# Performance work log

Hardware: AMD Instinct MI355X
Metric: run time of the kernel (lower is better)

Reference implementation:

```python
import jax, jax.numpy as jnp
import numpy as np

V = 32000   # vocab.size
E = 512     # embed_dim
H = 512     # hidden_dim
L = 2       # num_layers
W = 32      # window_size
S = 512     # seq_len
B = 8       # batch


def setup_inputs() -> dict:
    key = jax.random.key(0)
    ks = jax.random.split(key, 2 + 4 * L)
    bound = 1.0 / np.sqrt(H)
    inp = {
        "encoder_input": jax.random.randint(ks[0], (S, B), 0, V),
        "embed_table": jax.random.normal(ks[1], (V, E), jnp.float32),
    }
    for l in range(L):
        in_dim = E if l == 0 else H
        k = ks[2 + 4 * l: 6 + 4 * l]
        inp[f"w_ih_{l}"] = jax.random.uniform(k[0], (4 * H, in_dim), jnp.float32, -bound, bound)
        inp[f"w_hh_{l}"] = jax.random.uniform(k[1], (4 * H, H), jnp.float32, -bound, bound)
        inp[f"b_ih_{l}"] = jax.random.uniform(k[2], (4 * H,), jnp.float32, -bound, bound)
        inp[f"b_hh_{l}"] = jax.random.uniform(k[3], (4 * H,), jnp.float32, -bound, bound)
    return inp


def _lstm_layer(x, mask, w_ih, w_hh, b_ih, b_hh):
    # x: [T, N, D]; mask: [T, N, 1]. Masked steps keep (h, c), so every window
    # effectively starts from a zero state at its first valid position (same as
    # running a fresh LSTM on each window, torch gate order i,f,g,o).
    N = x.shape[1]
    Hd = w_hh.shape[1]
    bias = b_ih + b_hh

    def step(carry, inp_):
        h, c = carry
        xt, mt = inp_
        gates = xt @ w_ih.T + h @ w_hh.T + bias  # [N, 4H]
        i, f, g, o = jnp.split(gates, 4, axis=-1)
        i = jax.nn.sigmoid(i)
        f = jax.nn.sigmoid(f)
        g = jnp.tanh(g)
        o = jax.nn.sigmoid(o)
        c_new = f * c + i * g
        h_new = o * jnp.tanh(c_new)
        h = jnp.where(mt, h_new, h)
        c = jnp.where(mt, c_new, c)
        return (h, c), h

    z = jnp.zeros((N, Hd), x.dtype)
    (h, _), ys = jax.lax.scan(step, (z, z), (x, mask))
    return ys, h


def reference(encoder_input, embed_table,
              w_ih_0, w_hh_0, b_ih_0, b_hh_0,
              w_ih_1, w_hh_1, b_ih_1, b_hh_1):
    emb = embed_table[encoder_input]              # [S, B, E]
    T = W + 1
    # window position t for target index i is i - W + t (invalid when < 0)
    pos = jnp.arange(S)[None, :] - W + jnp.arange(T)[:, None]  # [T, S]
    valid = pos >= 0
    windows = emb[jnp.clip(pos, 0)]               # [T, S, B, E]
    x = windows.reshape(T, S * B, E)
    mask = jnp.broadcast_to(valid[:, :, None], (T, S, B)).reshape(T, S * B, 1)

    params = [(w_ih_0, w_hh_0, b_ih_0, b_hh_0), (w_ih_1, w_hh_1, b_ih_1, b_hh_1)]
    h = None
    for (wi, wh, bi, bh) in params:
        x, h = _lstm_layer(x, mask, wi, wh, bi, bh)
    # original takes encoder_output at the last window position == final hidden
    return h.reshape(S, B, H)
```

## Files before the change

### kernel.cpp

```cpp
#include <hip/hip_runtime.h>
#include <stdint.h>

#define NROWS 4096
#define HDIM  512
#define GDIM  2048
#define WWIN  32

typedef __attribute__((ext_vector_type(8))) short short8;
typedef __attribute__((ext_vector_type(4))) float f32x4;

__device__ __forceinline__ unsigned short f2bf(float x){
  union { float f; unsigned int u; } v; v.f = x;
  unsigned int u = v.u + 0x7fffu + ((v.u >> 16) & 1u);
  return (unsigned short)(u >> 16);
}

__device__ __forceinline__ void gld16(const void* g, void* l){
  __builtin_amdgcn_global_load_lds(
      (const __attribute__((address_space(1))) unsigned int*)g,
      (__attribute__((address_space(3))) unsigned int*)l, 16, 0, 0);
}

__device__ __forceinline__ float sigm(float x){ return 1.f/(1.f + __expf(-x)); }
__device__ __forceinline__ float tanh_f(float x){ return 1.f - 2.f/(1.f + __expf(2.f*x)); }

__device__ __forceinline__ void gemm_tile_db(
    const char* A0, const char* A1, const char* Bsrc,
    int ldbB, int nk, int r0, int c0,
    char* smem, int wr, int wc, int lane, f32x4 acc[4][4])
{
  const int tid = threadIdx.x;
  const int oo0 = tid * 16;
  const int srow = oo0 >> 7;
  const int scb  = oo0 & 127;
  const size_t aOff = (size_t)(r0 + srow) * 1024 + scb;
  const size_t bOff = (size_t)(c0 + srow) * (size_t)ldbB + scb;

  auto STAGE = [&](int kk, int buf){
    const char* Ap = (kk < 8) ? A0 : A1;
    const size_t kbA = (size_t)(kk & 7) * 128;
    const size_t kbB = (size_t)kk * 128;
    char* AsB = smem + buf * 16384;
    char* BsB = smem + 32768 + buf * 16384;
    #pragma unroll
    for (int i = 0; i < 4; ++i){
      const size_t rstep = (size_t)i * 32;
      gld16(Ap   + aOff + rstep * 1024          + kbA, AsB + i*4096 + oo0);
      gld16(Bsrc + bOff + rstep * (size_t)ldbB  + kbB, BsB + i*4096 + oo0);
    }
  };

  STAGE(0, 0);
  __syncthreads();

  const int lr = lane & 15;
  const int lk = (lane >> 4) * 8;

  for (int kk = 0; kk < nk; ++kk){
    const int cur = kk & 1;
    if (kk + 1 < nk) STAGE(kk + 1, cur ^ 1);

    const unsigned short* As = (const unsigned short*)(smem + cur*16384);
    const unsigned short* Bs = (const unsigned short*)(smem + 32768 + cur*16384);
    short8 a[2][4], b[2][4];
    #pragma unroll
    for (int h = 0; h < 2; ++h){
      const int k32 = h * 32;
      #pragma unroll
      for (int m = 0; m < 4; ++m)
        a[h][m] = *(const short8*)(As + (64*wr + 16*m + lr)*64 + k32 + lk);
      #pragma unroll
      for (int n = 0; n < 4; ++n)
        b[h][n] = *(const short8*)(Bs + (64*wc + 16*n + lr)*64 + k32 + lk);
    }
    __builtin_amdgcn_s_setprio(1);
    #pragma unroll
    for (int h = 0; h < 2; ++h)
      #pragma unroll
      for (int m = 0; m < 4; ++m)
        #pragma unroll
        for (int n = 0; n < 4; ++n)
          acc[m][n] = __builtin_amdgcn_mfma_f32_16x16x32_bf16(a[h][m], b[h][n], acc[m][n], 0, 0, 0);
    __builtin_amdgcn_s_setprio(0);

    __syncthreads();
  }
}

__global__ void __launch_bounds__(256) prep_weights(
    const float* wih0, const float* whh0, const float* bih0, const float* bhh0,
    const float* wih1, const float* whh1, const float* bih1, const float* bhh1,
    unsigned short* BrIh0, unsigned short* Br0, unsigned short* Br1,
    float* bias0r, float* br1)
{
  const int j = blockIdx.x;
  const int g = j & 3, hd = j >> 2;
  const int r = g*512 + hd;
  for (int k = threadIdx.x; k < 512; k += 256){
    BrIh0[(size_t)j*512 + k]      = f2bf(wih0[(size_t)r*512 + k]);
    Br0  [(size_t)j*512 + k]      = f2bf(whh0[(size_t)r*512 + k]);
    Br1  [(size_t)j*1024 + k]     = f2bf(wih1[(size_t)r*512 + k]);
    Br1  [(size_t)j*1024 + 512+k] = f2bf(whh1[(size_t)r*512 + k]);
  }
  if (threadIdx.x == 0){
    bias0r[j] = bih0[r] + bhh0[r];
    br1[j]    = bih1[r] + bhh1[r];
  }
}

__global__ void __launch_bounds__(256) gather_embed(const int* enc, const float* tbl,
                                                    unsigned short* E)
{
  const int n = blockIdx.x;
  const int idx = enc[n];
  const float* src = tbl + (size_t)idx * 512;
  unsigned short* dst = E + (size_t)n * 512;
  for (int e = threadIdx.x; e < 512; e += 256) dst[e] = f2bf(src[e]);
}

__global__ void __launch_bounds__(256) p0_gemm(const unsigned short* E,
                                               const unsigned short* BrIh0,
                                               const float* bias0r, float* P0)
{
  __shared__ __align__(16) char smem[65536];
  const int tid  = threadIdx.x;
  const int lane = tid & 63, wid = tid >> 6;
  const int wr = wid >> 1, wc = wid & 1;
  const int bid = blockIdx.x;
  const int r0 = (bid >> 4) * 128, c0 = (bid & 15) * 128;
  f32x4 acc[4][4] = {};
  gemm_tile_db((const char*)E, nullptr, (const char*)BrIh0, 1024, 8,
               r0, c0, smem, wr, wc, lane, acc);
  #pragma unroll
  for (int m = 0; m < 4; ++m){
    const int rowb = r0 + 64*wr + 16*m + ((lane >> 4) << 2);
    #pragma unroll
    for (int n = 0; n < 4; ++n){
      const int colb = c0 + 64*wc + 16*n + (lane & 15);
      const float bs = bias0r[colb];
      #pragma unroll
      for (int r = 0; r < 4; ++r)
        P0[(size_t)(rowb + r)*GDIM + colb] = acc[m][n][r] + bs;
    }
  }
}

__global__ void __launch_bounds__(512, 2) step_kernel(
    unsigned short* h0, unsigned short* h1, float* c0b, float* c1b,
    const unsigned short* Br0, const unsigned short* Br1,
    const float* P0, const float* br1, float* out, int tau, int bidOff)
{
  extern __shared__ __align__(16) char smem[];

  const int x = blockIdx.x & 7, kq = blockIdx.x >> 3;
  int wk;
  if (gridDim.x == 256) wk = ((kq & 1) << 7) + x * 16 + (kq >> 1);
  else                  wk = x * 16 + kq;
  wk += bidOff;

  const bool L1 = (wk >= 128);
  const int t  = L1 ? (tau - 1) : tau;
  const int pr = (tau + 1) & 1, pw = tau & 1;
  const int lb = L1 ? (wk - 128) : wk;
  const int r0  = (lb >> 3) * 256;
  const int c0v = (lb & 7) * 256;

  const int tid  = threadIdx.x;
  const int lane = tid & 63;
  const int wid  = tid >> 6;
  const int wm = wid >> 2, wn = wid & 3;
  const int lr = lane & 15, sl = lane >> 4;

  const unsigned short* hA0 = h0 + (size_t)pr * (NROWS*HDIM);
  const unsigned short* hA1 = h1 + (size_t)pr * (NROWS*HDIM);
  const char* Bp  = (const char*)(L1 ? Br1 : Br0);
  const int  ldbB = L1 ? 2048 : 1024;
  const int  nkt  = L1 ? 32 : 16;

  const int srow  = tid >> 2;
  const int sbyte = ((tid & 3) ^ ((tid >> 3) & 3)) << 4;
  const int ph    = (sl ^ ((lr >> 1) & 3)) << 4;
  const int laneA = (wm*128 + lr) * 64 + ph;
  const int laneB = (wn*64  + lr) * 64 + ph;

  auto STAGE_A = [&](int kt2, int c){
    const char* Ap; int kB;
    if (!L1 || kt2 < 16){ Ap = (const char*)hA0; kB = kt2 * 64; }
    else                { Ap = (const char*)hA1; kB = (kt2 - 16) * 64; }
    gld16(Ap + (size_t)(r0 + c*128 + srow) * 1024 + kB + sbyte,
          smem + (size_t)(kt2 & 3) * 32768 + c*8192 + tid*16);
  };
  auto STAGE_B = [&](int kt2, int c){
    gld16(Bp + (size_t)(c0v + c*128 + srow) * (size_t)ldbB + kt2*64 + sbyte,
          smem + (size_t)(kt2 & 3) * 32768 + 16384 + c*8192 + tid*16);
  };

  f32x4 acc[8][4] = {};

  STAGE_A(0,0); STAGE_A(0,1); STAGE_B(0,0); STAGE_B(0,1);
  STAGE_A(1,0); STAGE_A(1,1); STAGE_B(1,0); STAGE_B(1,1);
  asm volatile("s_waitcnt vmcnt(4)" ::: "memory");
  __builtin_amdgcn_s_barrier();

  for (int kt = 0; kt < nkt; ++kt){
    const char* bufp = smem + (size_t)(kt & 3) * 32768;
    const bool st = (kt + 2) < nkt;
    short8 a0[4], a1[4], b[4];

    #pragma unroll
    for (int m = 0; m < 4; ++m) a0[m] = *(const short8*)(bufp + laneA + m*1024);
    #pragma unroll
    for (int n = 0; n < 4; ++n) b[n]  = *(const short8*)(bufp + 16384 + laneB + n*1024);
    if (st){ STAGE_A(kt+2, 0); STAGE_A(kt+2, 1); }
    __builtin_amdgcn_s_barrier();
    asm volatile("s_waitcnt lgkmcnt(0)" ::: "memory");
    __builtin_amdgcn_sched_barrier(0);
    __builtin_amdgcn_s_setprio(1);
    #pragma unroll
    for (int m = 0; m < 4; ++m)
      #pragma unroll
      for (int n = 0; n < 4; ++n)
        acc[m][n] = __builtin_amdgcn_mfma_f32_16x16x32_bf16(a0[m], b[n], acc[m][n], 0, 0, 0);
    __builtin_amdgcn_s_setprio(0);
    __builtin_amdgcn_s_barrier();

    #pragma unroll
    for (int m = 0; m < 4; ++m) a1[m] = *(const short8*)(bufp + laneA + (4+m)*1024);
    if (st){
      STAGE_B(kt+2, 0); STAGE_B(kt+2, 1);
      asm volatile("s_waitcnt vmcnt(4)" ::: "memory");
    } else {
      asm volatile("s_waitcnt vmcnt(0)" ::: "memory");
    }
    __builtin_amdgcn_s_barrier();
    asm volatile("s_waitcnt lgkmcnt(0)" ::: "memory");
    __builtin_amdgcn_sched_barrier(0);
    __builtin_amdgcn_s_setprio(1);
    #pragma unroll
    for (int m = 0; m < 4; ++m)
      #pragma unroll
      for (int n = 0; n < 4; ++n)
        acc[4+m][n] = __builtin_amdgcn_mfma_f32_16x16x32_bf16(a1[m], b[n], acc[4+m][n], 0, 0, 0);
    __builtin_amdgcn_s_setprio(0);
    __builtin_amdgcn_s_barrier();
  }

  float* GLDS = (float*)smem;
  const int GST = 68;
  float* cbuf = L1 ? c1b : c0b;
  unsigned short* hw = (L1 ? h1 : h0) + (size_t)pw * (NROWS*HDIM);
  const bool finalStep = (L1 && t == 32);

  for (int pass = 0; pass < 4; ++pass){
    __syncthreads();
    if (wn == pass){
      #pragma unroll
      for (int m = 0; m < 8; ++m){
        const int rowb = wm*128 + m*16 + (sl << 2);
        #pragma unroll
        for (int n = 0; n < 4; ++n){
          const int colb = n*16 + lr;
          const f32x4 v = acc[m][n];
          #pragma unroll
          for (int r = 0; r < 4; ++r)
            GLDS[(rowb + r)*GST + colb] = v[r];
        }
      }
    }
    __syncthreads();
    #pragma unroll
    for (int it = 0; it < 8; ++it){
      const int cid = it*512 + tid;
      const int row = cid >> 4;
      const int l   = cid & 15;
      const int rowg = r0 + row;
      const int hd   = (c0v >> 2) + pass*16 + l;
      float4 gv = *(const float4*)&GLDS[row*GST + 4*l];
      float gi = gv.x, gf = gv.y, gg = gv.z, go = gv.w;
      const int s  = rowg >> 3;
      const int bb = rowg & 7;
      const int pos = s - WWIN + t;
      if (!L1){
        const int p0r = (pos < 0 ? 0 : pos)*8 + bb;
        float4 pv = *(const float4*)&P0[(size_t)p0r*GDIM + 4*hd];
        gi += pv.x; gf += pv.y; gg += pv.z; go += pv.w;
      } else {
        float4 bv = *(const float4*)&br1[4*hd];
        gi += bv.x; gf += bv.y; gg += bv.z; go += bv.w;
      }
      const size_t sidx = (size_t)rowg*HDIM + hd;
      float cp = cbuf[sidx];
      float i_ = sigm(gi), f_ = sigm(gf), g_ = tanh_f(gg), o_ = sigm(go);
      float cn = f_*cp + i_*g_;
      float hn = o_*tanh_f(cn);
      if (pos < 0){ cn = 0.f; hn = 0.f; }
      cbuf[sidx] = cn;
      if (finalStep) out[sidx] = hn;
      else           hw[sidx]  = f2bf(hn);
    }
  }
}

extern "C" void kernel_launch(void* const* d_in, const int* in_sizes, int n_in,
                              void* d_out, int out_size, void* d_ws, size_t ws_size,
                              hipStream_t stream)
{
  const int*   enc  = (const int*)d_in[0];
  const float* tbl  = (const float*)d_in[1];
  const float* wih0 = (const float*)d_in[2];
  const float* whh0 = (const float*)d_in[3];
  const float* bih0 = (const float*)d_in[4];
  const float* bhh0 = (const float*)d_in[5];
  const float* wih1 = (const float*)d_in[6];
  const float* whh1 = (const float*)d_in[7];
  const float* bih1 = (const float*)d_in[8];
  const float* bhh1 = (const float*)d_in[9];
  float* out = (float*)d_out;

  char* ws = (char*)d_ws;
  size_t off = 0;
  auto alloc = [&](size_t bytes){
    char* p = ws + off; off += (bytes + 255) & ~(size_t)255; return p;
  };
  unsigned short* E     = (unsigned short*)alloc((size_t)NROWS*512*2);
  unsigned short* BrIh0 = (unsigned short*)alloc((size_t)GDIM*512*2);
  unsigned short* Br0   = (unsigned short*)alloc((size_t)GDIM*512*2);
  unsigned short* Br1   = (unsigned short*)alloc((size_t)GDIM*1024*2);
  float* bias0r = (float*)alloc(GDIM*4);
  float* br1    = (float*)alloc(GDIM*4);
  float* P0     = (float*)alloc((size_t)NROWS*GDIM*4);
  unsigned short* h0 = (unsigned short*)alloc((size_t)2*NROWS*HDIM*2);
  unsigned short* h1 = (unsigned short*)alloc((size_t)2*NROWS*HDIM*2);
  float* c0 = (float*)alloc((size_t)NROWS*HDIM*4);
  float* c1 = (float*)alloc((size_t)NROWS*HDIM*4);
  if (off > ws_size) return;

  (void)hipFuncSetAttribute(reinterpret_cast<const void*>(step_kernel),
                            hipFuncAttributeMaxDynamicSharedMemorySize, 131072);

  hipMemsetAsync(h0, 0, (size_t)33554432, stream);

  prep_weights<<<2048, 256, 0, stream>>>(wih0, whh0, bih0, bhh0,
                                         wih1, whh1, bih1, bhh1,
                                         BrIh0, Br0, Br1, bias0r, br1);
  gather_embed<<<4096, 256, 0, stream>>>(enc, tbl, E);
  p0_gemm<<<512, 256, 0, stream>>>(E, BrIh0, bias0r, P0);
  for (int tau = 0; tau <= 33; ++tau){
    const int grid = (tau == 0 || tau == 33) ? 128 : 256;
    const int boff = (tau == 33) ? 128 : 0;
    step_kernel<<<grid, 512, 131072, stream>>>(h0, h1, c0, c1, Br0, Br1,
                                               P0, br1, out, tau, boff);
  }
}
```

Baseline: 1.714 ms.

## Fuse recurrent timesteps into one cooperative persistent kernel with grid barrier

Replaces the 34 per-timestep step_kernel launches with a single cooperative persistent kernel. It steps through all timesteps behind a custom atomic grid barrier and keeps the cell state in registers instead of global memory. The precomputed layer-0 input projection P0 is also stored in bf16 instead of fp32, halving its write and read traffic. The aim is to remove launch gaps and c-state traffic, at the cost of spin-barrier overhead, extra register pressure and reduced precision in P0.

```diff
diff --git a/kernel.cpp b/kernel.cpp
--- a/kernel.cpp
+++ b/kernel.cpp
@@ -14,6 +14,9 @@
   unsigned int u = v.u + 0x7fffu + ((v.u >> 16) & 1u);
   return (unsigned short)(u >> 16);
 }
+__device__ __forceinline__ float bf2f(unsigned short u){
+  union { unsigned int u; float f; } v; v.u = ((unsigned int)u) << 16; return v.f;
+}
 
 __device__ __forceinline__ void gld16(const void* g, void* l){
   __builtin_amdgcn_global_load_lds(
@@ -23,6 +26,24 @@
 
 __device__ __forceinline__ float sigm(float x){ return 1.f/(1.f + __expf(-x)); }
 __device__ __forceinline__ float tanh_f(float x){ return 1.f - 2.f/(1.f + __expf(2.f*x)); }
+
+__device__ __forceinline__ void grid_sync(unsigned* bar, unsigned target){
+  __syncthreads();
+  if (threadIdx.x == 0){
+    __builtin_amdgcn_fence(__ATOMIC_RELEASE, "agent");
+    unsigned arrived = __hip_atomic_fetch_add(&bar[0], 1u, __ATOMIC_RELAXED,
+                                              __HIP_MEMORY_SCOPE_AGENT);
+    if (arrived == gridDim.x - 1){
+      __hip_atomic_store(&bar[0], 0u, __ATOMIC_RELAXED, __HIP_MEMORY_SCOPE_AGENT);
+      __hip_atomic_store(&bar[1], target, __ATOMIC_RELEASE, __HIP_MEMORY_SCOPE_AGENT);
+    } else {
+      while (__hip_atomic_load(&bar[1], __ATOMIC_RELAXED, __HIP_MEMORY_SCOPE_AGENT) < target)
+        __builtin_amdgcn_s_sleep(8);
+    }
+    __builtin_amdgcn_fence(__ATOMIC_ACQUIRE, "agent");
+  }
+  __syncthreads();
+}
 
 __device__ __forceinline__ void gemm_tile_db(
     const char* A0, const char* A1, const char* Bsrc,
@@ -120,7 +141,8 @@
 
 __global__ void __launch_bounds__(256) p0_gemm(const unsigned short* E,
                                                const unsigned short* BrIh0,
-                                               const float* bias0r, float* P0)
+                                               const float* bias0r,
+                                               unsigned short* P0)
 {
   __shared__ __align__(16) char smem[65536];
   const int tid  = threadIdx.x;
@@ -140,15 +162,179 @@
       const float bs = bias0r[colb];
       #pragma unroll
       for (int r = 0; r < 4; ++r)
-        P0[(size_t)(rowb + r)*GDIM + colb] = acc[m][n][r] + bs;
-    }
+        P0[(size_t)(rowb + r)*GDIM + colb] = f2bf(acc[m][n][r] + bs);
+    }
+  }
+}
+
+__global__ void __launch_bounds__(512, 2) persist_kernel(
+    unsigned short* h0, unsigned short* h1,
+    const unsigned short* Br0, const unsigned short* Br1,
+    const unsigned short* P0, const float* br1, float* out, unsigned* bar)
+{
+  extern __shared__ __align__(16) char smem[];
+
+  const int x = blockIdx.x & 7, kq = blockIdx.x >> 3;
+  const int wk = ((kq & 1) << 7) + x * 16 + (kq >> 1);
+  const bool L1 = (wk >= 128);
+  const int lb = L1 ? (wk - 128) : wk;
+  const int r0  = (lb >> 3) * 256;
+  const int c0v = (lb & 7) * 256;
+
+  const int tid  = threadIdx.x;
+  const int lane = tid & 63, wid = tid >> 6;
+  const int wm = wid >> 2, wn = wid & 3;
+  const int lr = lane & 15, sl = lane >> 4;
+
+  const int srow  = tid >> 2;
+  const int sbyte = ((tid & 3) ^ ((tid >> 3) & 3)) << 4;
+  const int ph    = (sl ^ ((lr >> 1) & 3)) << 4;
+  const int laneA = (wm*128 + lr) * 64 + ph;
+  const int laneB = (wn*64  + lr) * 64 + ph;
+
+  const char* Bp  = (const char*)(L1 ? Br1 : Br0);
+  const int  ldbB = L1 ? 2048 : 1024;
+  const int  nkt  = L1 ? 32 : 16;
+
+  float creg[4][8];
+  #pragma unroll
+  for (int p = 0; p < 4; ++p)
+    #pragma unroll
+    for (int i = 0; i < 8; ++i) creg[p][i] = 0.f;
+
+  for (int tau = 0; tau <= 33; ++tau){
+    const bool active = L1 ? (tau >= 1) : (tau <= 32);
+    if (active){
+      const int t  = L1 ? (tau - 1) : tau;
+      const int pr = (tau + 1) & 1, pw = tau & 1;
+      const unsigned short* hA0 = h0 + (size_t)pr * (NROWS*HDIM);
+      const unsigned short* hA1 = h1 + (size_t)pr * (NROWS*HDIM);
+
+      auto STAGE_A = [&](int kt2, int c){
+        const char* Ap; int kB;
+        if (!L1 || kt2 < 16){ Ap = (const char*)hA0; kB = kt2 * 64; }
+        else                { Ap = (const char*)hA1; kB = (kt2 - 16) * 64; }
+        gld16(Ap + (size_t)(r0 + c*128 + srow) * 1024 + kB + sbyte,
+              smem + (size_t)(kt2 & 3) * 32768 + c*8192 + tid*16);
+      };
+      auto STAGE_B = [&](int kt2, int c){
+        gld16(Bp + (size_t)(c0v + c*128 + srow) * (size_t)ldbB + kt2*64 + sbyte,
+              smem + (size_t)(kt2 & 3) * 32768 + 16384 + c*8192 + tid*16);
+      };
+
+      f32x4 acc[8][4] = {};
+
+      STAGE_A(0,0); STAGE_A(0,1); STAGE_B(0,0); STAGE_B(0,1);
+      STAGE_A(1,0); STAGE_A(1,1); STAGE_B(1,0); STAGE_B(1,1);
+      asm volatile("s_waitcnt vmcnt(4)" ::: "memory");
+      __builtin_amdgcn_s_barrier();
+
+      for (int kt = 0; kt < nkt; ++kt){
+        const char* bufp = smem + (size_t)(kt & 3) * 32768;
+        const bool st = (kt + 2) < nkt;
+        short8 a0[4], a1[4], b[4];
+
+        #pragma unroll
+        for (int m = 0; m < 4; ++m) a0[m] = *(const short8*)(bufp + laneA + m*1024);
+        #pragma unroll
+        for (int n = 0; n < 4; ++n) b[n]  = *(const short8*)(bufp + 16384 + laneB + n*1024);
+        if (st){ STAGE_A(kt+2, 0); STAGE_A(kt+2, 1); }
+        __builtin_amdgcn_s_barrier();
+        asm volatile("s_waitcnt lgkmcnt(0)" ::: "memory");
+        __builtin_amdgcn_sched_barrier(0);
+        __builtin_amdgcn_s_setprio(1);
+        #pragma unroll
+        for (int m = 0; m < 4; ++m)
+          #pragma unroll
+          for (int n = 0; n < 4; ++n)
+            acc[m][n] = __builtin_amdgcn_mfma_f32_16x16x32_bf16(a0[m], b[n], acc[m][n], 0, 0, 0);
+        __builtin_amdgcn_s_setprio(0);
+        __builtin_amdgcn_s_barrier();
+
+        #pragma unroll
+        for (int m = 0; m < 4; ++m) a1[m] = *(const short8*)(bufp + laneA + (4+m)*1024);
+        if (st){
+          STAGE_B(kt+2, 0); STAGE_B(kt+2, 1);
+          asm volatile("s_waitcnt vmcnt(4)" ::: "memory");
+        } else {
+          asm volatile("s_waitcnt vmcnt(0)" ::: "memory");
+        }
+        __builtin_amdgcn_s_barrier();
+        asm volatile("s_waitcnt lgkmcnt(0)" ::: "memory");
+        __builtin_amdgcn_sched_barrier(0);
+        __builtin_amdgcn_s_setprio(1);
+        #pragma unroll
+        for (int m = 0; m < 4; ++m)
+          #pragma unroll
+          for (int n = 0; n < 4; ++n)
+            acc[4+m][n] = __builtin_amdgcn_mfma_f32_16x16x32_bf16(a1[m], b[n], acc[4+m][n], 0, 0, 0);
+        __builtin_amdgcn_s_setprio(0);
+        __builtin_amdgcn_s_barrier();
+      }
+
+      float* GLDS = (float*)smem;
+      const int GST = 68;
+      unsigned short* hw = (L1 ? h1 : h0) + (size_t)pw * (NROWS*HDIM);
+      const bool finalStep = (L1 && t == 32);
+
+      #pragma unroll
+      for (int pass = 0; pass < 4; ++pass){
+        __syncthreads();
+        if (wn == pass){
+          #pragma unroll
+          for (int m = 0; m < 8; ++m){
+            const int rowb = wm*128 + m*16 + (sl << 2);
+            #pragma unroll
+            for (int n = 0; n < 4; ++n){
+              const int colb = n*16 + lr;
+              const f32x4 v = acc[m][n];
+              #pragma unroll
+              for (int r = 0; r < 4; ++r)
+                GLDS[(rowb + r)*GST + colb] = v[r];
+            }
+          }
+        }
+        __syncthreads();
+        #pragma unroll
+        for (int it = 0; it < 8; ++it){
+          const int cid = it*512 + tid;
+          const int row = cid >> 4;
+          const int l   = cid & 15;
+          const int rowg = r0 + row;
+          const int hd   = (c0v >> 2) + pass*16 + l;
+          float4 gv = *(const float4*)&GLDS[row*GST + 4*l];
+          float gi = gv.x, gf = gv.y, gg = gv.z, go = gv.w;
+          const int s  = rowg >> 3;
+          const int bb = rowg & 7;
+          const int pos = s - WWIN + t;
+          if (!L1){
+            const int p0r = (pos < 0 ? 0 : pos)*8 + bb;
+            const ushort4 pv = *(const ushort4*)&P0[(size_t)p0r*GDIM + 4*hd];
+            gi += bf2f(pv.x); gf += bf2f(pv.y); gg += bf2f(pv.z); go += bf2f(pv.w);
+          } else {
+            float4 bv = *(const float4*)&br1[4*hd];
+            gi += bv.x; gf += bv.y; gg += bv.z; go += bv.w;
+          }
+          float cp = creg[pass][it];
+          float i_ = sigm(gi), f_ = sigm(gf), g_ = tanh_f(gg), o_ = sigm(go);
+          float cn = f_*cp + i_*g_;
+          float hn = o_*tanh_f(cn);
+          if (pos < 0){ cn = 0.f; hn = 0.f; }
+          creg[pass][it] = cn;
+          const size_t sidx = (size_t)rowg*HDIM + hd;
+          if (finalStep) out[sidx] = hn;
+          else           hw[sidx]  = f2bf(hn);
+        }
+      }
+    }
+    grid_sync(bar, (unsigned)(tau + 1));
   }
 }
 
 __global__ void __launch_bounds__(512, 2) step_kernel(
     unsigned short* h0, unsigned short* h1, float* c0b, float* c1b,
     const unsigned short* Br0, const unsigned short* Br1,
-    const float* P0, const float* br1, float* out, int tau, int bidOff)
+    const unsigned short* P0, const float* br1, float* out, int tau, int bidOff)
 {
   extern __shared__ __align__(16) char smem[];
 
@@ -282,8 +468,8 @@
       const int pos = s - WWIN + t;
       if (!L1){
         const int p0r = (pos < 0 ? 0 : pos)*8 + bb;
-        float4 pv = *(const float4*)&P0[(size_t)p0r*GDIM + 4*hd];
-        gi += pv.x; gf += pv.y; gg += pv.z; go += pv.w;
+        const ushort4 pv = *(const ushort4*)&P0[(size_t)p0r*GDIM + 4*hd];
+        gi += bf2f(pv.x); gf += bf2f(pv.y); gg += bf2f(pv.z); go += bf2f(pv.w);
       } else {
         float4 bv = *(const float4*)&br1[4*hd];
         gi += bv.x; gf += bv.y; gg += bv.z; go += bv.w;
@@ -328,27 +514,44 @@
   unsigned short* Br1   = (unsigned short*)alloc((size_t)GDIM*1024*2);
   float* bias0r = (float*)alloc(GDIM*4);
   float* br1    = (float*)alloc(GDIM*4);
-  float* P0     = (float*)alloc((size_t)NROWS*GDIM*4);
+  unsigned short* P0 = (unsigned short*)alloc((size_t)NROWS*GDIM*2);
   unsigned short* h0 = (unsigned short*)alloc((size_t)2*NROWS*HDIM*2);
   unsigned short* h1 = (unsigned short*)alloc((size_t)2*NROWS*HDIM*2);
   float* c0 = (float*)alloc((size_t)NROWS*HDIM*4);
   float* c1 = (float*)alloc((size_t)NROWS*HDIM*4);
+  unsigned* bar = (unsigned*)alloc(256);
   if (off > ws_size) return;
 
+  (void)hipFuncSetAttribute(reinterpret_cast<const void*>(persist_kernel),
+                            hipFuncAttributeMaxDynamicSharedMemorySize, 131072);
   (void)hipFuncSetAttribute(reinterpret_cast<const void*>(step_kernel),
                             hipFuncAttributeMaxDynamicSharedMemorySize, 131072);
 
-  hipMemsetAsync(h0, 0, (size_t)33554432, stream);
+  hipMemsetAsync(h0, 0, (size_t)33554688, stream);
 
   prep_weights<<<2048, 256, 0, stream>>>(wih0, whh0, bih0, bhh0,
                                          wih1, whh1, bih1, bhh1,
                                          BrIh0, Br0, Br1, bias0r, br1);
   gather_embed<<<4096, 256, 0, stream>>>(enc, tbl, E);
   p0_gemm<<<512, 256, 0, stream>>>(E, BrIh0, bias0r, P0);
-  for (int tau = 0; tau <= 33; ++tau){
-    const int grid = (tau == 0 || tau == 33) ? 128 : 256;
-    const int boff = (tau == 33) ? 128 : 0;
-    step_kernel<<<grid, 512, 131072, stream>>>(h0, h1, c0, c1, Br0, Br1,
-                                               P0, br1, out, tau, boff);
-  }
-}
+
+  int occ = 0;
+  hipError_t oe = hipOccupancyMaxActiveBlocksPerMultiprocessor(
+      &occ, reinterpret_cast<const void*>(persist_kernel), 512, 131072);
+  bool coop = (oe == hipSuccess && occ >= 1);
+  if (coop){
+    void* kargs[] = {&h0, &h1, &Br0, &Br1, &P0, &br1, &out, &bar};
+    hipError_t le = hipLaunchCooperativeKernel(
+        reinterpret_cast<const void*>(persist_kernel),
+        dim3(256), dim3(512), kargs, 131072, stream);
+    if (le != hipSuccess) coop = false;
+  }
+  if (!coop){
+    for (int tau = 0; tau <= 33; ++tau){
+      const int grid = (tau == 0 || tau == 33) ? 128 : 256;
+      const int boff = (tau == 33) ? 128 : 0;
+      step_kernel<<<grid, 512, 131072, stream>>>(h0, h1, c0, c1, Br0, Br1,
+                                                 P0, br1, out, tau, boff);
+    }
+  }
+}
```

Result: no change. 1.741 ms (+1.6%).
